# Optimization experiments

Measured on AMD Instinct MI355X. Metric: run time of the kernel, lower is better.

Reference implementation:

```python
import jax, jax.numpy as jnp
import numpy as np

# --- gate hyperparameters (from init config) ---
DIM = 2048
N_EXPERTS = 256
TOPK = 8
N_GROUPS = 8
TOPK_GROUPS = 4
GROUP_TOPK = 2
ROUTE_SCALE = 2.5
T_TOKENS = 32768
NEG_INF = jnp.float32(-1e30)


def setup_inputs() -> dict:
    key = jax.random.key(0)
    kx, kw, kb = jax.random.split(key, 3)
    x = jax.random.normal(kx, (T_TOKENS, DIM), dtype=jnp.float32)
    # nn.init.normal_(weight, std=0.006)
    weight = 0.006 * jax.random.normal(kw, (N_EXPERTS, DIM), dtype=jnp.float32)
    # bias buffer starts at zero but gets adjusted; use small nonzero values so it matters
    bias = 0.001 * jax.random.normal(kb, (N_EXPERTS,), dtype=jnp.float32)
    return {"x": x, "weight": weight, "bias": bias}


def reference(x, weight, bias):
    T = x.shape[0]
    # scores = sigmoid(x @ W^T)  -> (T, E)
    scores = jax.nn.sigmoid(jnp.einsum("td,ed->te", x, weight))
    biased = scores + bias.astype(scores.dtype)  # (T, E)

    # --- group-limited routing ---
    epg = N_EXPERTS // N_GROUPS
    bg = biased.reshape(T, N_GROUPS, epg)  # (T, G, E/G)
    # group score = sum of top-`GROUP_TOPK` biased scores within each group
    group_scores = jax.lax.top_k(bg, GROUP_TOPK)[0].sum(axis=-1)  # (T, G)
    top_groups = jax.lax.top_k(group_scores, TOPK_GROUPS)[1]  # (T, topk_groups)
    keep = jnp.zeros((T, N_GROUPS), dtype=bool).at[
        jnp.arange(T)[:, None], top_groups
    ].set(True)  # (T, G)
    biased = jnp.where(keep[:, :, None], bg, NEG_INF).reshape(T, N_EXPERTS)

    # --- final top-k over biased scores; weights from RAW sigmoid scores ---
    indices = jax.lax.top_k(biased, TOPK)[1]  # (T, topk) int32
    weights = jnp.take_along_axis(scores, indices, axis=1)  # (T, topk)
    weights = weights / jnp.maximum(
        weights.sum(axis=-1, keepdims=True), jnp.float32(1e-10)
    )
    weights = (weights * jnp.float32(ROUTE_SCALE)).astype(x.dtype)
    return weights, indices
```

## Files before the change

kernel.cpp:

```cpp
#include <hip/hip_runtime.h>
#include <math.h>

#define T_TOKENS 32768
#define DIM 2048
#define N_EXPERTS 256
#define N_GROUPS 8
#define EPG 32
#define TOPK 8
#define TOPK_GROUPS 4
#define ROUTE_SCALE 2.5f

#define BM 64
#define BK 32
#define KP 40
#define KITERS (DIM / BK)
#define W_SCALE 256.0f
#define INV_W_SCALE (1.0f / 256.0f)

typedef unsigned short u16;
typedef _Float16 f16x8 __attribute__((ext_vector_type(8)));
typedef float f32x4 __attribute__((ext_vector_type(4)));

__device__ __forceinline__ u16 f16_bits(_Float16 h) {
    union { _Float16 f; u16 u; } c; c.f = h; return c.u;
}

__global__ __launch_bounds__(256) void convert_w(
    const float* __restrict__ W, u16* __restrict__ Whi, u16* __restrict__ Wlo)
{
    const int i = blockIdx.x * 256 + threadIdx.x;
    const float x = W[i] * W_SCALE;
    const _Float16 hi = (_Float16)x;
    const _Float16 lo = (_Float16)(x - (float)hi);
    Whi[i] = f16_bits(hi);
    Wlo[i] = f16_bits(lo);
}

__global__ __launch_bounds__(512, 4) void fused_gate(
    const float* __restrict__ X,
    const u16* __restrict__ Whi, const u16* __restrict__ Wlo,
    const float* __restrict__ bias,
    float* __restrict__ out_w, float* __restrict__ out_i)
{
    __shared__ __align__(16) char smem[65536];
    u16* Ahi = (u16*)smem;
    u16* Alo = Ahi + BM * KP;
    u16* Bhi = Alo + BM * KP;
    u16* Blo = Bhi + N_EXPERTS * KP;
    float* Sc = (float*)smem;

    const int tid = threadIdx.x;
    const int m0 = blockIdx.x * BM;

    const int ar = tid >> 3;
    const int ac = (tid & 7) * 4;
    const int br = tid >> 2;
    const int bc = (tid & 3) * 8;

    const float* xa = X + (size_t)(m0 + ar) * DIM + ac;
    const u16* wh0 = Whi + br * DIM + bc;
    const u16* wh1 = Whi + (br + 128) * DIM + bc;
    const u16* wl0 = Wlo + br * DIM + bc;
    const u16* wl1 = Wlo + (br + 128) * DIM + bc;

    const int lane = tid & 63;
    const int wave = tid >> 6;
    const int wm = wave >> 2;
    const int wn = wave & 3;
    const int l16 = lane & 15;
    const int quad = lane >> 4;

    f32x4 acc[2][4];
    #pragma unroll
    for (int i = 0; i < 2; i++)
        #pragma unroll
        for (int j = 0; j < 4; j++) acc[i][j] = (f32x4){0.f, 0.f, 0.f, 0.f};

    float4 a0 = *(const float4*)(xa);
    uint4 h0 = *(const uint4*)(wh0);
    uint4 h1 = *(const uint4*)(wh1);
    uint4 l0 = *(const uint4*)(wl0);
    uint4 l1 = *(const uint4*)(wl1);

    for (int it = 0; it < KITERS; ++it) {
        __syncthreads();
        {
            ushort4 h, l;
            _Float16 t;
            t = (_Float16)a0.x; h.x = f16_bits(t); l.x = f16_bits((_Float16)(a0.x - (float)t));
            t = (_Float16)a0.y; h.y = f16_bits(t); l.y = f16_bits((_Float16)(a0.y - (float)t));
            t = (_Float16)a0.z; h.z = f16_bits(t); l.z = f16_bits((_Float16)(a0.z - (float)t));
            t = (_Float16)a0.w; h.w = f16_bits(t); l.w = f16_bits((_Float16)(a0.w - (float)t));
            *(ushort4*)&Ahi[ar * KP + ac] = h;
            *(ushort4*)&Alo[ar * KP + ac] = l;
        }
        *(uint4*)&Bhi[br * KP + bc] = h0;
        *(uint4*)&Bhi[(br + 128) * KP + bc] = h1;
        *(uint4*)&Blo[br * KP + bc] = l0;
        *(uint4*)&Blo[(br + 128) * KP + bc] = l1;
        __syncthreads();

        if (it + 1 < KITERS) {
            const int ko = (it + 1) * BK;
            a0 = *(const float4*)(xa + ko);
            h0 = *(const uint4*)(wh0 + ko);
            h1 = *(const uint4*)(wh1 + ko);
            l0 = *(const uint4*)(wl0 + ko);
            l1 = *(const uint4*)(wl1 + ko);
        }

        f16x8 fah[2], fal[2], fbh[4], fbl[4];
        #pragma unroll
        for (int i = 0; i < 2; i++) {
            const int mrow = wm * 32 + i * 16 + l16;
            fah[i] = *(const f16x8*)&Ahi[mrow * KP + quad * 8];
            fal[i] = *(const f16x8*)&Alo[mrow * KP + quad * 8];
        }
        #pragma unroll
        for (int j = 0; j < 4; j++) {
            const int nrow = wn * 64 + j * 16 + l16;
            fbh[j] = *(const f16x8*)&Bhi[nrow * KP + quad * 8];
            fbl[j] = *(const f16x8*)&Blo[nrow * KP + quad * 8];
        }
        #pragma unroll
        for (int i = 0; i < 2; i++)
            #pragma unroll
            for (int j = 0; j < 4; j++) {
                acc[i][j] = __builtin_amdgcn_mfma_f32_16x16x32_f16(fah[i], fbh[j], acc[i][j], 0, 0, 0);
                acc[i][j] = __builtin_amdgcn_mfma_f32_16x16x32_f16(fah[i], fbl[j], acc[i][j], 0, 0, 0);
                acc[i][j] = __builtin_amdgcn_mfma_f32_16x16x32_f16(fal[i], fbh[j], acc[i][j], 0, 0, 0);
            }
    }

    float bv[4];
    #pragma unroll
    for (int j = 0; j < 4; j++) bv[j] = bias[wn * 64 + j * 16 + l16];

    __syncthreads();
    #pragma unroll
    for (int i = 0; i < 2; i++)
        #pragma unroll
        for (int j = 0; j < 4; j++)
            #pragma unroll
            for (int r = 0; r < 4; r++) {
                const int trow = wm * 32 + i * 16 + quad * 4 + r;
                const int e = wn * 64 + j * 16 + l16;
                const float logit = acc[i][j][r] * INV_W_SCALE;
                const float s = 1.f / (1.f + expf(-logit));
                Sc[trow * N_EXPERTS + e] = s + bv[j];
            }
    __syncthreads();

    if (tid < 64) {
        const float* row = Sc + tid * N_EXPERTS;

        float gs[N_GROUPS];
        #pragma unroll
        for (int g = 0; g < N_GROUPS; g++) {
            float m1 = -INFINITY, m2 = -INFINITY;
            #pragma unroll
            for (int jj = 0; jj < EPG; jj++) {
                const float v = row[g * EPG + ((tid + jj) & (EPG - 1))];
                if (v > m1) { m2 = m1; m1 = v; }
                else if (v > m2) { m2 = v; }
            }
            gs[g] = m1 + m2;
        }
        unsigned keep = 0;
        #pragma unroll
        for (int g = 0; g < N_GROUPS; g++) {
            int cnt = 0;
            #pragma unroll
            for (int h = 0; h < N_GROUPS; h++)
                if (gs[h] > gs[g] || (gs[h] == gs[g] && h < g)) cnt++;
            if (cnt < TOPK_GROUPS) keep |= (1u << g);
        }
        float tv[TOPK]; int ti[TOPK];
        #pragma unroll
        for (int i = 0; i < TOPK; i++) { tv[i] = -INFINITY; ti[i] = 0x7fffffff; }
        for (int g = 0; g < N_GROUPS; g++) {
            if (!(keep & (1u << g))) continue;
            #pragma unroll 4
            for (int jj = 0; jj < EPG; jj++) {
                const int e = g * EPG + ((tid + jj) & (EPG - 1));
                const float v = row[e];
                if (v > tv[TOPK - 1] || (v == tv[TOPK - 1] && e < ti[TOPK - 1])) {
                    float cv = v; int ce = e;
                    #pragma unroll
                    for (int s = 0; s < TOPK; s++) {
                        const bool b = (cv > tv[s]) || (cv == tv[s] && ce < ti[s]);
                        if (b) {
                            const float t1 = tv[s]; tv[s] = cv; cv = t1;
                            const int t2 = ti[s]; ti[s] = ce; ce = t2;
                        }
                    }
                }
            }
        }
        float w[TOPK], sum = 0.f;
        #pragma unroll
        for (int i = 0; i < TOPK; i++) {
            w[i] = row[ti[i]] - bias[ti[i]];
            sum += w[i];
        }
        const float scale = ROUTE_SCALE / fmaxf(sum, 1e-10f);
        const size_t t = (size_t)m0 + tid;
        #pragma unroll
        for (int i = 0; i < TOPK; i++) {
            out_w[t * TOPK + i] = w[i] * scale;
            out_i[t * TOPK + i] = (float)ti[i];
        }
    }
}

extern "C" void kernel_launch(void* const* d_in, const int* in_sizes, int n_in,
                              void* d_out, int out_size, void* d_ws, size_t ws_size,
                              hipStream_t stream)
{
    const float* x = (const float*)d_in[0];
    const float* w = (const float*)d_in[1];
    const float* b = (const float*)d_in[2];

    u16* whi = (u16*)d_ws;
    u16* wlo = whi + (size_t)N_EXPERTS * DIM;

    float* out_w = (float*)d_out;
    float* out_i = (float*)d_out + (size_t)T_TOKENS * TOPK;

    convert_w<<<(N_EXPERTS * DIM) / 256, 256, 0, stream>>>(w, whi, wlo);
    fused_gate<<<T_TOKENS / BM, 512, 0, stream>>>(x, whi, wlo, b, out_w, out_i);
}
```

Measured before the change: 604.6 us.

## Load MFMA operands directly from global memory, dropping LDS staging and barriers

The GEMM main loop no longer stages X and W tiles through shared memory. Each lane now loads its MFMA fragments straight from global memory, splitting X into fp16 hi/lo in registers and prefetching the next X slice, which removes the two barriers per k-iteration and the LDS traffic. In exchange, each W element is fetched by every wave that uses it (the two wm waves) and by every block, and the per-lane 16-byte loads are strided across rows, so coalescing is weaker and more load traffic goes through L2.

```diff
diff --git a/kernel.cpp b/kernel.cpp
--- a/kernel.cpp
+++ b/kernel.cpp
@@ -12,7 +12,6 @@
 
 #define BM 64
 #define BK 32
-#define KP 40
 #define KITERS (DIM / BK)
 #define W_SCALE 256.0f
 #define INV_W_SCALE (1.0f / 256.0f)
@@ -36,32 +35,28 @@
     Wlo[i] = f16_bits(lo);
 }
 
+__device__ __forceinline__ void split8(const float4 p, const float4 q,
+                                       f16x8* hi, f16x8* lo)
+{
+    const float v[8] = {p.x, p.y, p.z, p.w, q.x, q.y, q.z, q.w};
+    #pragma unroll
+    for (int k = 0; k < 8; k++) {
+        const _Float16 h = (_Float16)v[k];
+        (*hi)[k] = h;
+        (*lo)[k] = (_Float16)(v[k] - (float)h);
+    }
+}
+
 __global__ __launch_bounds__(512, 4) void fused_gate(
     const float* __restrict__ X,
     const u16* __restrict__ Whi, const u16* __restrict__ Wlo,
     const float* __restrict__ bias,
     float* __restrict__ out_w, float* __restrict__ out_i)
 {
-    __shared__ __align__(16) char smem[65536];
-    u16* Ahi = (u16*)smem;
-    u16* Alo = Ahi + BM * KP;
-    u16* Bhi = Alo + BM * KP;
-    u16* Blo = Bhi + N_EXPERTS * KP;
-    float* Sc = (float*)smem;
+    __shared__ float Sc[BM * N_EXPERTS];
 
     const int tid = threadIdx.x;
     const int m0 = blockIdx.x * BM;
-
-    const int ar = tid >> 3;
-    const int ac = (tid & 7) * 4;
-    const int br = tid >> 2;
-    const int bc = (tid & 3) * 8;
-
-    const float* xa = X + (size_t)(m0 + ar) * DIM + ac;
-    const u16* wh0 = Whi + br * DIM + bc;
-    const u16* wh1 = Whi + (br + 128) * DIM + bc;
-    const u16* wl0 = Wlo + br * DIM + bc;
-    const u16* wl1 = Wlo + (br + 128) * DIM + bc;
 
     const int lane = tid & 63;
     const int wave = tid >> 6;
@@ -70,58 +65,46 @@
     const int l16 = lane & 15;
     const int quad = lane >> 4;
 
+    const float* xa0 = X + (size_t)(m0 + wm * 32 + l16) * DIM + quad * 8;
+    const float* xa1 = xa0 + 16 * DIM;
+    const u16* wbh = Whi + (size_t)(wn * 64 + l16) * DIM + quad * 8;
+    const u16* wbl = Wlo + (size_t)(wn * 64 + l16) * DIM + quad * 8;
+
     f32x4 acc[2][4];
     #pragma unroll
     for (int i = 0; i < 2; i++)
         #pragma unroll
         for (int j = 0; j < 4; j++) acc[i][j] = (f32x4){0.f, 0.f, 0.f, 0.f};
 
-    float4 a0 = *(const float4*)(xa);
-    uint4 h0 = *(const uint4*)(wh0);
-    uint4 h1 = *(const uint4*)(wh1);
-    uint4 l0 = *(const uint4*)(wl0);
-    uint4 l1 = *(const uint4*)(wl1);
-
+    float4 a00 = *(const float4*)(xa0);
+    float4 a01 = *(const float4*)(xa0 + 4);
+    float4 a10 = *(const float4*)(xa1);
+    float4 a11 = *(const float4*)(xa1 + 4);
+
+    #pragma unroll 2
     for (int it = 0; it < KITERS; ++it) {
-        __syncthreads();
-        {
-            ushort4 h, l;
-            _Float16 t;
-            t = (_Float16)a0.x; h.x = f16_bits(t); l.x = f16_bits((_Float16)(a0.x - (float)t));
-            t = (_Float16)a0.y; h.y = f16_bits(t); l.y = f16_bits((_Float16)(a0.y - (float)t));
-            t = (_Float16)a0.z; h.z = f16_bits(t); l.z = f16_bits((_Float16)(a0.z - (float)t));
-            t = (_Float16)a0.w; h.w = f16_bits(t); l.w = f16_bits((_Float16)(a0.w - (float)t));
-            *(ushort4*)&Ahi[ar * KP + ac] = h;
-            *(ushort4*)&Alo[ar * KP + ac] = l;
-        }
-        *(uint4*)&Bhi[br * KP + bc] = h0;
-        *(uint4*)&Bhi[(br + 128) * KP + bc] = h1;
-        *(uint4*)&Blo[br * KP + bc] = l0;
-        *(uint4*)&Blo[(br + 128) * KP + bc] = l1;
-        __syncthreads();
-
+        const int cur = it * BK;
+
+        f16x8 fbh[4], fbl[4];
+        #pragma unroll
+        for (int j = 0; j < 4; j++) {
+            fbh[j] = *(const f16x8*)(wbh + (size_t)j * 16 * DIM + cur);
+            fbl[j] = *(const f16x8*)(wbl + (size_t)j * 16 * DIM + cur);
+        }
+
+        float4 n00, n01, n10, n11;
         if (it + 1 < KITERS) {
-            const int ko = (it + 1) * BK;
-            a0 = *(const float4*)(xa + ko);
-            h0 = *(const uint4*)(wh0 + ko);
-            h1 = *(const uint4*)(wh1 + ko);
-            l0 = *(const uint4*)(wl0 + ko);
-            l1 = *(const uint4*)(wl1 + ko);
-        }
-
-        f16x8 fah[2], fal[2], fbh[4], fbl[4];
-        #pragma unroll
-        for (int i = 0; i < 2; i++) {
-            const int mrow = wm * 32 + i * 16 + l16;
-            fah[i] = *(const f16x8*)&Ahi[mrow * KP + quad * 8];
-            fal[i] = *(const f16x8*)&Alo[mrow * KP + quad * 8];
-        }
-        #pragma unroll
-        for (int j = 0; j < 4; j++) {
-            const int nrow = wn * 64 + j * 16 + l16;
-            fbh[j] = *(const f16x8*)&Bhi[nrow * KP + quad * 8];
-            fbl[j] = *(const f16x8*)&Blo[nrow * KP + quad * 8];
-        }
+            const int nxt = cur + BK;
+            n00 = *(const float4*)(xa0 + nxt);
+            n01 = *(const float4*)(xa0 + nxt + 4);
+            n10 = *(const float4*)(xa1 + nxt);
+            n11 = *(const float4*)(xa1 + nxt + 4);
+        }
+
+        f16x8 fah[2], fal[2];
+        split8(a00, a01, &fah[0], &fal[0]);
+        split8(a10, a11, &fah[1], &fal[1]);
+
         #pragma unroll
         for (int i = 0; i < 2; i++)
             #pragma unroll
@@ -130,13 +113,14 @@
                 acc[i][j] = __builtin_amdgcn_mfma_f32_16x16x32_f16(fah[i], fbl[j], acc[i][j], 0, 0, 0);
                 acc[i][j] = __builtin_amdgcn_mfma_f32_16x16x32_f16(fal[i], fbh[j], acc[i][j], 0, 0, 0);
             }
+
+        if (it + 1 < KITERS) { a00 = n00; a01 = n01; a10 = n10; a11 = n11; }
     }
 
     float bv[4];
     #pragma unroll
     for (int j = 0; j < 4; j++) bv[j] = bias[wn * 64 + j * 16 + l16];
 
-    __syncthreads();
     #pragma unroll
     for (int i = 0; i < 2; i++)
         #pragma unroll
```

Measured after the change: 732.2 us. 21.1% more time.
